# Kernel optimization log

Hardware: AMD Instinct MI355X
Metric: run time of the kernel (lower is better)

The kernel has to match this reference:

```python
import jax, jax.numpy as jnp
import numpy as np

D_MODEL = 1024
D_HEAD = 64  # d_model / num_heads
NEG_INF = -1e9  # matches torch code's -1000000000.0 additive mask


def setup_inputs() -> dict:
    key = jax.random.key(0)
    ks = jax.random.split(key, 9)
    B, S = 4, 4096
    scale = 0.02
    return {
        "q": jax.random.normal(ks[0], (B, S, D_MODEL), dtype=jnp.float32),
        "k": jax.random.normal(ks[1], (B, S, D_MODEL), dtype=jnp.float32),
        "v": jax.random.normal(ks[2], (B, S, D_MODEL), dtype=jnp.float32),
        "WQ_w": jax.random.normal(ks[3], (D_HEAD, D_MODEL), dtype=jnp.float32) * scale,
        "WQ_b": jax.random.normal(ks[4], (D_HEAD,), dtype=jnp.float32) * scale,
        "WK_w": jax.random.normal(ks[5], (D_HEAD, D_MODEL), dtype=jnp.float32) * scale,
        "WK_b": jax.random.normal(ks[6], (D_HEAD,), dtype=jnp.float32) * scale,
        "WV_w": jax.random.normal(ks[7], (D_HEAD, D_MODEL), dtype=jnp.float32) * scale,
        "WV_b": jax.random.normal(ks[8], (D_HEAD,), dtype=jnp.float32) * scale,
    }


def reference(q, k, v, WQ_w, WQ_b, WK_w, WK_b, WV_w, WV_b):
    # Linear projections (torch nn.Linear: x @ W.T + b)
    qh = jnp.einsum("bsd,hd->bsh", q, WQ_w) + WQ_b  # [B,S,64]
    kh = jnp.einsum("bsd,hd->bsh", k, WK_w) + WK_b
    vh = jnp.einsum("bsd,hd->bsh", v, WV_w) + WV_b
    # Scaled dot-product scores [B,S,S]
    scores = jnp.einsum("bqh,bkh->bqk", qh, kh) / np.sqrt(D_HEAD).astype(np.float32)
    # Causal additive mask: upper triangle (j > i) gets -1e9
    S = scores.shape[-1]
    causal = jnp.triu(jnp.ones((S, S), dtype=scores.dtype), k=1) * NEG_INF
    scores = scores + causal
    attn = jax.nn.softmax(scores, axis=-1)
    out = jnp.einsum("bqk,bkh->bqh", attn, vh)  # [B,S,64]
    # Dropout is identity in eval mode (deterministic reference)
    return out
```

## Files before the change

### kernel.cpp

```cpp
#include <hip/hip_runtime.h>

#define SEQ 4096
#define DM  1024
#define DH  64
#define NB  4
#define SLOTS_PER_B 288

typedef __attribute__((ext_vector_type(4))) float  f32x4;
typedef __attribute__((ext_vector_type(8))) __bf16 bf16x8;

__device__ __forceinline__ unsigned short f2bf(float f) {
    unsigned int u = __float_as_uint(f);
    u += 0x7FFFu + ((u >> 16) & 1u);
    return (unsigned short)(u >> 16);
}

__device__ __forceinline__ f32x4 mfma_bf16(bf16x8 a, bf16x8 b, f32x4 c) {
    return __builtin_amdgcn_mfma_f32_16x16x32_bf16(a, b, c, 0, 0, 0);
}

__global__ __launch_bounds__(256) void proj_kernel(
    const float* __restrict__ xq, const float* __restrict__ xk, const float* __restrict__ xv,
    const float* __restrict__ Wq, const float* __restrict__ bq,
    const float* __restrict__ Wk, const float* __restrict__ bk,
    const float* __restrict__ Wv, const float* __restrict__ bv,
    unsigned short* __restrict__ qh, unsigned short* __restrict__ kh,
    unsigned short* __restrict__ vhT)
{
    __shared__ unsigned short x_tile[64][72];
    __shared__ unsigned short w_tile[64][72];

    const int which = blockIdx.y;
    const float* X  = (which == 0) ? xq : (which == 1) ? xk : xv;
    const float* W  = (which == 0) ? Wq : (which == 1) ? Wk : Wv;
    const float* Bb = (which == 0) ? bq : (which == 1) ? bk : bv;

    const int m0   = blockIdx.x * 64;
    const int t    = threadIdx.x;
    const int wv   = t >> 6;
    const int lane = t & 63;
    const int quad = lane >> 4;
    const int l16  = lane & 15;
    const int sr   = t >> 2;
    const int sc   = (t & 3) << 4;

    f32x4 acc[4];
#pragma unroll
    for (int i = 0; i < 4; ++i) acc[i] = f32x4{0.f, 0.f, 0.f, 0.f};

    const float* xg = X + (size_t)(m0 + sr) * DM + sc;
    const float* wg = W + (size_t)sr * DM + sc;

    f32x4 xr[4], wr[4];
#pragma unroll
    for (int i = 0; i < 4; ++i) { xr[i] = *(const f32x4*)(xg + i * 4); wr[i] = *(const f32x4*)(wg + i * 4); }

    for (int kc = 0; kc < DM; kc += 64) {
        __syncthreads();
#pragma unroll
        for (int i = 0; i < 4; ++i) {
            *(ushort4*)&x_tile[sr][sc + i * 4] =
                make_ushort4(f2bf(xr[i][0]), f2bf(xr[i][1]), f2bf(xr[i][2]), f2bf(xr[i][3]));
            *(ushort4*)&w_tile[sr][sc + i * 4] =
                make_ushort4(f2bf(wr[i][0]), f2bf(wr[i][1]), f2bf(wr[i][2]), f2bf(wr[i][3]));
        }
        __syncthreads();
        if (kc + 64 < DM) {
            const float* xn = xg + kc + 64;
            const float* wn = wg + kc + 64;
#pragma unroll
            for (int i = 0; i < 4; ++i) { xr[i] = *(const f32x4*)(xn + i * 4); wr[i] = *(const f32x4*)(wn + i * 4); }
        }
#pragma unroll
        for (int ks = 0; ks < 2; ++ks) {
            bf16x8 a = *(const bf16x8*)&x_tile[wv * 16 + l16][ks * 32 + quad * 8];
#pragma unroll
            for (int nt = 0; nt < 4; ++nt) {
                bf16x8 b = *(const bf16x8*)&w_tile[nt * 16 + l16][ks * 32 + quad * 8];
                acc[nt] = mfma_bf16(a, b, acc[nt]);
            }
        }
    }

    __syncthreads();
#pragma unroll
    for (int nt = 0; nt < 4; ++nt) {
        float bias = Bb[nt * 16 + l16];
#pragma unroll
        for (int r = 0; r < 4; ++r)
            x_tile[wv * 16 + quad * 4 + r][nt * 16 + l16] = f2bf(acc[nt][r] + bias);
    }
    __syncthreads();

    if (which < 2) {
        unsigned short* out = (which == 0) ? qh : kh;
        unsigned short* og  = out + (size_t)(m0 + sr) * DH + sc;
        *(int4*)og       = *(const int4*)&x_tile[sr][sc];
        *(int4*)(og + 8) = *(const int4*)&x_tile[sr][sc + 8];
    } else {
        const int bb = m0 >> 12;
        const int s0 = m0 & 4095;
        const int h  = sr;
        const int r0 = sc;
        __align__(16) unsigned short tmp[16];
#pragma unroll
        for (int i = 0; i < 16; ++i) tmp[i] = x_tile[r0 + i][h];
        unsigned short* og = vhT + (size_t)bb * DH * SEQ + (size_t)h * SEQ + (s0 + r0);
        *(int4*)og       = *(const int4*)&tmp[0];
        *(int4*)(og + 8) = *(const int4*)&tmp[8];
    }
}

__global__ __launch_bounds__(256) void attn_split_kernel(
    const unsigned short* __restrict__ qh, const unsigned short* __restrict__ kh,
    const unsigned short* __restrict__ vhT,
    float* __restrict__ pO, float* __restrict__ pm, float* __restrict__ pl)
{
    const int chunk = blockIdx.x;
    const int qt    = blockIdx.y;
    const int b     = blockIdx.z;
    const int nc    = (qt + 8) >> 3;
    if (chunk >= nc) return;

    const int g = qt >> 3, rr = qt & 7;
    const int slot = b * SLOTS_PER_B + 4 * g * (g + 1) + rr * (g + 1) + chunk;
    const int c0 = chunk * 8;
    const int c1 = min(c0 + 8, qt + 1);

    __shared__ unsigned short k_t[64][72];
    __shared__ unsigned short v_t[64][72];
    __shared__ unsigned short qp[64][72];

    const int t    = threadIdx.x;
    const int wv   = t >> 6;
    const int lane = t & 63;
    const int quad = lane >> 4;
    const int l16  = lane & 15;
    const int sr   = t >> 2;
    const int sc   = (t & 3) << 4;

    const size_t base = (size_t)b * SEQ * DH;

    {
        const unsigned short* gq = qh + base + (size_t)(qt * 64 + sr) * DH + sc;
        *(int4*)&qp[sr][sc]     = *(const int4*)gq;
        *(int4*)&qp[sr][sc + 8] = *(const int4*)(gq + 8);
    }
    __syncthreads();
    bf16x8 qfrag[2];
    qfrag[0] = *(const bf16x8*)&qp[wv * 16 + l16][quad * 8];
    qfrag[1] = *(const bf16x8*)&qp[wv * 16 + l16][32 + quad * 8];

    f32x4 o_acc[4];
#pragma unroll
    for (int i = 0; i < 4; ++i) o_acc[i] = f32x4{0.f, 0.f, 0.f, 0.f};
    float m_i[4], l_i[4];
#pragma unroll
    for (int r = 0; r < 4; ++r) { m_i[r] = -1e30f; l_i[r] = 0.f; }

    const int rowb = wv * 16 + quad * 4;

    for (int jt = c0; jt < c1; ++jt) {
        __syncthreads();
        {
            const unsigned short* kg = kh + base + (size_t)(jt * 64 + sr) * DH + sc;
            *(int4*)&k_t[sr][sc]     = *(const int4*)kg;
            *(int4*)&k_t[sr][sc + 8] = *(const int4*)(kg + 8);
            const unsigned short* vg = vhT + (size_t)b * DH * SEQ + (size_t)sr * SEQ + (jt * 64 + sc);
            *(int4*)&v_t[sr][sc]     = *(const int4*)vg;
            *(int4*)&v_t[sr][sc + 8] = *(const int4*)(vg + 8);
        }
        __syncthreads();

        f32x4 s_acc[4];
#pragma unroll
        for (int i = 0; i < 4; ++i) s_acc[i] = f32x4{0.f, 0.f, 0.f, 0.f};
#pragma unroll
        for (int ks = 0; ks < 2; ++ks) {
#pragma unroll
            for (int nt = 0; nt < 4; ++nt) {
                bf16x8 bfr = *(const bf16x8*)&k_t[nt * 16 + l16][ks * 32 + quad * 8];
                s_acc[nt] = mfma_bf16(qfrag[ks], bfr, s_acc[nt]);
            }
        }

        const bool diag = (jt == qt);
#pragma unroll
        for (int nt = 0; nt < 4; ++nt) {
            const int col = nt * 16 + l16;
#pragma unroll
            for (int r = 0; r < 4; ++r) {
                float sv = s_acc[nt][r] * 0.125f;
                if (diag && (col > rowb + r)) sv = -1e30f;
                s_acc[nt][r] = sv;
            }
        }

        float mx[4];
#pragma unroll
        for (int r = 0; r < 4; ++r)
            mx[r] = fmaxf(fmaxf(s_acc[0][r], s_acc[1][r]), fmaxf(s_acc[2][r], s_acc[3][r]));
#pragma unroll
        for (int off = 1; off < 16; off <<= 1)
#pragma unroll
            for (int r = 0; r < 4; ++r)
                mx[r] = fmaxf(mx[r], __shfl_xor(mx[r], off, 64));

        float alpha[4];
#pragma unroll
        for (int r = 0; r < 4; ++r) {
            float mn = fmaxf(m_i[r], mx[r]);
            alpha[r] = __expf(m_i[r] - mn);
            m_i[r]   = mn;
        }

        float rs[4] = {0.f, 0.f, 0.f, 0.f};
#pragma unroll
        for (int nt = 0; nt < 4; ++nt)
#pragma unroll
            for (int r = 0; r < 4; ++r) {
                float p = __expf(s_acc[nt][r] - m_i[r]);
                s_acc[nt][r] = p;
                rs[r] += p;
            }
#pragma unroll
        for (int off = 1; off < 16; off <<= 1)
#pragma unroll
            for (int r = 0; r < 4; ++r)
                rs[r] += __shfl_xor(rs[r], off, 64);
#pragma unroll
        for (int r = 0; r < 4; ++r) l_i[r] = l_i[r] * alpha[r] + rs[r];

#pragma unroll
        for (int nt = 0; nt < 4; ++nt)
#pragma unroll
            for (int r = 0; r < 4; ++r)
                qp[rowb + r][nt * 16 + l16] = f2bf(s_acc[nt][r]);

#pragma unroll
        for (int nt = 0; nt < 4; ++nt)
#pragma unroll
            for (int r = 0; r < 4; ++r)
                o_acc[nt][r] *= alpha[r];

#pragma unroll
        for (int ks = 0; ks < 2; ++ks) {
            bf16x8 pa = *(const bf16x8*)&qp[wv * 16 + l16][ks * 32 + quad * 8];
#pragma unroll
            for (int nt = 0; nt < 4; ++nt) {
                bf16x8 vb = *(const bf16x8*)&v_t[nt * 16 + l16][ks * 32 + quad * 8];
                o_acc[nt] = mfma_bf16(pa, vb, o_acc[nt]);
            }
        }
    }

    float* po = pO + (size_t)slot * 4096;
#pragma unroll
    for (int nt = 0; nt < 4; ++nt)
#pragma unroll
        for (int r = 0; r < 4; ++r)
            po[(rowb + r) * 64 + nt * 16 + l16] = o_acc[nt][r];
    if (l16 == 0) {
#pragma unroll
        for (int r = 0; r < 4; ++r) {
            pm[slot * 64 + rowb + r] = m_i[r];
            pl[slot * 64 + rowb + r] = l_i[r];
        }
    }
}

__global__ __launch_bounds__(256) void attn_merge_kernel(
    const float* __restrict__ pO, const float* __restrict__ pm, const float* __restrict__ pl,
    float* __restrict__ out)
{
    const int qt = blockIdx.x;
    const int b  = blockIdx.y;
    const int nc = (qt + 8) >> 3;
    const int g = qt >> 3, rr = qt & 7;
    const int s0 = b * SLOTS_PER_B + 4 * g * (g + 1) + rr * (g + 1);

    const int t   = threadIdx.x;
    const int row = t >> 2;
    const int c0  = (t & 3) << 4;

    float mstar = -1e30f;
    for (int c = 0; c < nc; ++c)
        mstar = fmaxf(mstar, pm[(s0 + c) * 64 + row]);

    f32x4 acc[4];
#pragma unroll
    for (int i = 0; i < 4; ++i) acc[i] = f32x4{0.f, 0.f, 0.f, 0.f};
    float lsum = 0.f;

    for (int c = 0; c < nc; ++c) {
        const float w = __expf(pm[(s0 + c) * 64 + row] - mstar);
        lsum += w * pl[(s0 + c) * 64 + row];
        const float* p = pO + (size_t)(s0 + c) * 4096 + row * 64 + c0;
#pragma unroll
        for (int i = 0; i < 4; ++i) {
            f32x4 v = *(const f32x4*)(p + i * 4);
            acc[i] += w * v;
        }
    }

    const float inv = 1.0f / lsum;
    float* og = out + (size_t)b * SEQ * DH + (size_t)(qt * 64 + row) * DH + c0;
#pragma unroll
    for (int i = 0; i < 4; ++i)
        *(f32x4*)(og + i * 4) = acc[i] * inv;
}

extern "C" void kernel_launch(void* const* d_in, const int* in_sizes, int n_in,
                              void* d_out, int out_size, void* d_ws, size_t ws_size,
                              hipStream_t stream)
{
    (void)in_sizes; (void)n_in; (void)out_size; (void)ws_size;
    const float* q  = (const float*)d_in[0];
    const float* k  = (const float*)d_in[1];
    const float* v  = (const float*)d_in[2];
    const float* Wq = (const float*)d_in[3];
    const float* bq = (const float*)d_in[4];
    const float* Wk = (const float*)d_in[5];
    const float* bk = (const float*)d_in[6];
    const float* Wv = (const float*)d_in[7];
    const float* bv = (const float*)d_in[8];
    float* out = (float*)d_out;

    unsigned short* qh  = (unsigned short*)d_ws;
    unsigned short* kh  = qh + (size_t)NB * SEQ * DH;
    unsigned short* vhT = kh + (size_t)NB * SEQ * DH;
    float* pO = (float*)(vhT + (size_t)NB * SEQ * DH);
    float* pm = pO + (size_t)NB * SLOTS_PER_B * 4096;
    float* pl = pm + (size_t)NB * SLOTS_PER_B * 64;

    proj_kernel<<<dim3(NB * SEQ / 64, 3), 256, 0, stream>>>(
        q, k, v, Wq, bq, Wk, bk, Wv, bv, qh, kh, vhT);
    attn_split_kernel<<<dim3(8, SEQ / 64, NB), 256, 0, stream>>>(qh, kh, vhT, pO, pm, pl);
    attn_merge_kernel<<<dim3(SEQ / 64, NB), 256, 0, stream>>>(pO, pm, pl, out);
}
```

Measured before the change: 280.5 us.

## Prepack bf16 weights and double-buffer projection GEMM with async LDS loads

Adds a small pre-kernel that converts the three projection weight matrices to bf16 once, already laid out in MFMA fragment order, into scratch space that the attention partials reuse later. The projection kernel then streams these weight fragments straight into LDS with global_load_lds into double-buffered tiles, and keeps X fp32 loads several chunks ahead in registers. This removes the redundant per-block weight fp32 loads and conversions and overlaps memory with MFMA. In exchange it adds an extra kernel launch, manual waitcnt/barrier bookkeeping, and higher LDS and register use.

```diff
diff --git a/kernel.cpp b/kernel.cpp
--- a/kernel.cpp
+++ b/kernel.cpp
@@ -15,25 +15,56 @@
     return (unsigned short)(u >> 16);
 }
 
+__device__ __forceinline__ unsigned short bfc(float f) {
+    __bf16 h = (__bf16)f;
+    return __builtin_bit_cast(unsigned short, h);
+}
+
 __device__ __forceinline__ f32x4 mfma_bf16(bf16x8 a, bf16x8 b, f32x4 c) {
     return __builtin_amdgcn_mfma_f32_16x16x32_bf16(a, b, c, 0, 0, 0);
 }
 
+__device__ __forceinline__ void gload_lds16(const void* g, void* l) {
+    __builtin_amdgcn_global_load_lds(
+        (const __attribute__((address_space(1))) void*)g,
+        (__attribute__((address_space(3))) void*)l, 16, 0, 0);
+}
+
+__global__ __launch_bounds__(256) void wprep_kernel(
+    const float* __restrict__ Wq, const float* __restrict__ Wk, const float* __restrict__ Wv,
+    unsigned short* __restrict__ Wf)
+{
+    const int which = blockIdx.y;
+    const int kc    = blockIdx.x;
+    const float* W  = (which == 0) ? Wq : (which == 1) ? Wk : Wv;
+    unsigned short* out = Wf + (size_t)which * 65536 + (size_t)kc * 4096;
+    const int t = threadIdx.x;
+#pragma unroll
+    for (int s = t; s < 512; s += 256) {
+        const int ks = s >> 8, nt = (s >> 6) & 3, ln = s & 63;
+        const int qd = ln >> 4, l = ln & 15;
+        const float* src = W + (size_t)(nt * 16 + l) * DM + kc * 64 + ks * 32 + qd * 8;
+        f32x4 v0 = *(const f32x4*)src;
+        f32x4 v1 = *(const f32x4*)(src + 4);
+        *(ushort4*)(out + (size_t)s * 8)     = make_ushort4(bfc(v0[0]), bfc(v0[1]), bfc(v0[2]), bfc(v0[3]));
+        *(ushort4*)(out + (size_t)s * 8 + 4) = make_ushort4(bfc(v1[0]), bfc(v1[1]), bfc(v1[2]), bfc(v1[3]));
+    }
+}
+
 __global__ __launch_bounds__(256) void proj_kernel(
     const float* __restrict__ xq, const float* __restrict__ xk, const float* __restrict__ xv,
-    const float* __restrict__ Wq, const float* __restrict__ bq,
-    const float* __restrict__ Wk, const float* __restrict__ bk,
-    const float* __restrict__ Wv, const float* __restrict__ bv,
+    const unsigned short* __restrict__ Wf,
+    const float* __restrict__ bq, const float* __restrict__ bk, const float* __restrict__ bv,
     unsigned short* __restrict__ qh, unsigned short* __restrict__ kh,
     unsigned short* __restrict__ vhT)
 {
-    __shared__ unsigned short x_tile[64][72];
-    __shared__ unsigned short w_tile[64][72];
+    __shared__ unsigned short x_t[2][64][72];
+    __shared__ unsigned short wfb[2][4096];
 
     const int which = blockIdx.y;
     const float* X  = (which == 0) ? xq : (which == 1) ? xk : xv;
-    const float* W  = (which == 0) ? Wq : (which == 1) ? Wk : Wv;
     const float* Bb = (which == 0) ? bq : (which == 1) ? bk : bv;
+    const unsigned short* Wg = Wf + (size_t)which * 65536;
 
     const int m0   = blockIdx.x * 64;
     const int t    = threadIdx.x;
@@ -49,54 +80,82 @@
     for (int i = 0; i < 4; ++i) acc[i] = f32x4{0.f, 0.f, 0.f, 0.f};
 
     const float* xg = X + (size_t)(m0 + sr) * DM + sc;
-    const float* wg = W + (size_t)sr * DM + sc;
-
-    f32x4 xr[4], wr[4];
-#pragma unroll
-    for (int i = 0; i < 4; ++i) { xr[i] = *(const f32x4*)(xg + i * 4); wr[i] = *(const f32x4*)(wg + i * 4); }
-
-    for (int kc = 0; kc < DM; kc += 64) {
-        __syncthreads();
-#pragma unroll
-        for (int i = 0; i < 4; ++i) {
-            *(ushort4*)&x_tile[sr][sc + i * 4] =
-                make_ushort4(f2bf(xr[i][0]), f2bf(xr[i][1]), f2bf(xr[i][2]), f2bf(xr[i][3]));
-            *(ushort4*)&w_tile[sr][sc + i * 4] =
-                make_ushort4(f2bf(wr[i][0]), f2bf(wr[i][1]), f2bf(wr[i][2]), f2bf(wr[i][3]));
-        }
-        __syncthreads();
-        if (kc + 64 < DM) {
-            const float* xn = xg + kc + 64;
-            const float* wn = wg + kc + 64;
-#pragma unroll
-            for (int i = 0; i < 4; ++i) { xr[i] = *(const f32x4*)(xn + i * 4); wr[i] = *(const f32x4*)(wn + i * 4); }
-        }
-#pragma unroll
-        for (int ks = 0; ks < 2; ++ks) {
-            bf16x8 a = *(const bf16x8*)&x_tile[wv * 16 + l16][ks * 32 + quad * 8];
-#pragma unroll
-            for (int nt = 0; nt < 4; ++nt) {
-                bf16x8 b = *(const bf16x8*)&w_tile[nt * 16 + l16][ks * 32 + quad * 8];
-                acc[nt] = mfma_bf16(a, b, acc[nt]);
+
+    f32x4 xr[2][4];
+#pragma unroll
+    for (int i = 0; i < 4; ++i) xr[0][i] = *(const f32x4*)(xg + i * 4);
+#pragma unroll
+    for (int i = 0; i < 4; ++i) xr[1][i] = *(const f32x4*)(xg + 64 + i * 4);
+    {
+        const unsigned short* gs = Wg + (wv * 2) * 512 + lane * 8;
+        gload_lds16(gs,       &wfb[0][(wv * 2) * 512]);
+        gload_lds16(gs + 512, &wfb[0][(wv * 2) * 512 + 512]);
+    }
+    __builtin_amdgcn_sched_barrier(0);
+#pragma unroll
+    for (int i = 0; i < 4; ++i) {
+        f32x4 v = xr[0][i];
+        *(ushort4*)&x_t[0][sr][sc + i * 4] =
+            make_ushort4(bfc(v[0]), bfc(v[1]), bfc(v[2]), bfc(v[3]));
+    }
+#pragma unroll
+    for (int i = 0; i < 4; ++i) xr[0][i] = *(const f32x4*)(xg + 128 + i * 4);
+    asm volatile("s_waitcnt vmcnt(4)" ::: "memory");
+    asm volatile("s_waitcnt lgkmcnt(0)" ::: "memory");
+    __builtin_amdgcn_s_barrier();
+
+#pragma unroll
+    for (int j = 0; j < 16; ++j) {
+        const int cur = j & 1, nxt = cur ^ 1;
+        if (j + 1 < 16) {
+#pragma unroll
+            for (int i = 0; i < 4; ++i) {
+                f32x4 v = xr[nxt][i];
+                *(ushort4*)&x_t[nxt][sr][sc + i * 4] =
+                    make_ushort4(bfc(v[0]), bfc(v[1]), bfc(v[2]), bfc(v[3]));
             }
-        }
-    }
-
-    __syncthreads();
+            const unsigned short* gs = Wg + (size_t)(j + 1) * 4096 + (wv * 2) * 512 + lane * 8;
+            gload_lds16(gs,       &wfb[nxt][(wv * 2) * 512]);
+            gload_lds16(gs + 512, &wfb[nxt][(wv * 2) * 512 + 512]);
+        }
+        __builtin_amdgcn_sched_barrier(0);
+        if (j + 3 < 16) {
+            const float* xn = xg + (j + 3) * 64;
+#pragma unroll
+            for (int i = 0; i < 4; ++i) xr[nxt][i] = *(const f32x4*)(xn + i * 4);
+        }
+        bf16x8 a0 = *(const bf16x8*)&x_t[cur][wv * 16 + l16][quad * 8];
+        bf16x8 a1 = *(const bf16x8*)&x_t[cur][wv * 16 + l16][32 + quad * 8];
+#pragma unroll
+        for (int nt = 0; nt < 4; ++nt) {
+            bf16x8 b0 = *(const bf16x8*)&wfb[cur][(nt * 64 + lane) * 8];
+            acc[nt] = mfma_bf16(a0, b0, acc[nt]);
+        }
+#pragma unroll
+        for (int nt = 0; nt < 4; ++nt) {
+            bf16x8 b1 = *(const bf16x8*)&wfb[cur][((4 + nt) * 64 + lane) * 8];
+            acc[nt] = mfma_bf16(a1, b1, acc[nt]);
+        }
+        if (j < 13) asm volatile("s_waitcnt vmcnt(4)" ::: "memory");
+        else        asm volatile("s_waitcnt vmcnt(0)" ::: "memory");
+        asm volatile("s_waitcnt lgkmcnt(0)" ::: "memory");
+        __builtin_amdgcn_s_barrier();
+    }
+
 #pragma unroll
     for (int nt = 0; nt < 4; ++nt) {
         float bias = Bb[nt * 16 + l16];
 #pragma unroll
         for (int r = 0; r < 4; ++r)
-            x_tile[wv * 16 + quad * 4 + r][nt * 16 + l16] = f2bf(acc[nt][r] + bias);
+            x_t[0][wv * 16 + quad * 4 + r][nt * 16 + l16] = f2bf(acc[nt][r] + bias);
     }
     __syncthreads();
 
     if (which < 2) {
         unsigned short* out = (which == 0) ? qh : kh;
         unsigned short* og  = out + (size_t)(m0 + sr) * DH + sc;
-        *(int4*)og       = *(const int4*)&x_tile[sr][sc];
-        *(int4*)(og + 8) = *(const int4*)&x_tile[sr][sc + 8];
+        *(int4*)og       = *(const int4*)&x_t[0][sr][sc];
+        *(int4*)(og + 8) = *(const int4*)&x_t[0][sr][sc + 8];
     } else {
         const int bb = m0 >> 12;
         const int s0 = m0 & 4095;
@@ -104,7 +163,7 @@
         const int r0 = sc;
         __align__(16) unsigned short tmp[16];
 #pragma unroll
-        for (int i = 0; i < 16; ++i) tmp[i] = x_tile[r0 + i][h];
+        for (int i = 0; i < 16; ++i) tmp[i] = x_t[0][r0 + i][h];
         unsigned short* og = vhT + (size_t)bb * DH * SEQ + (size_t)h * SEQ + (s0 + r0);
         *(int4*)og       = *(const int4*)&tmp[0];
         *(int4*)(og + 8) = *(const int4*)&tmp[8];
@@ -332,9 +391,11 @@
     float* pO = (float*)(vhT + (size_t)NB * SEQ * DH);
     float* pm = pO + (size_t)NB * SLOTS_PER_B * 4096;
     float* pl = pm + (size_t)NB * SLOTS_PER_B * 64;
-
+    unsigned short* Wfb = (unsigned short*)pO;
+
+    wprep_kernel<<<dim3(16, 3), 256, 0, stream>>>(Wq, Wk, Wv, Wfb);
     proj_kernel<<<dim3(NB * SEQ / 64, 3), 256, 0, stream>>>(
-        q, k, v, Wq, bq, Wk, bk, Wv, bv, qh, kh, vhT);
+        q, k, v, Wfb, bq, bk, bv, qh, kh, vhT);
     attn_split_kernel<<<dim3(8, SEQ / 64, NB), 256, 0, stream>>>(qh, kh, vhT, pO, pm, pl);
     attn_merge_kernel<<<dim3(SEQ / 64, NB), 256, 0, stream>>>(pO, pm, pl, out);
 }
```

Result: no change. 283.3 us (+1.0%).

## Pre-swizzle bf16 weights and stream X directly into MFMA fragments in projection

Applied to the files above, without the earlier changes.

Adds a small kernel that converts the three projection weight matrices to bf16 once per call, laid out in MFMA fragment order, reusing the pO workspace before the split kernel overwrites it. The projection kernel then drops its shared-memory staging and barriers: each wave loads its X rows straight from global memory, converts them in registers, and reads the pre-swizzled weights directly. The merge kernel is split across four times more blocks, each thread handling one f32x4, to raise parallelism. In exchange, weight fragments are re-read from global or cache by every block, and it adds one more launch.

```diff
diff --git a/kernel.cpp b/kernel.cpp
--- a/kernel.cpp
+++ b/kernel.cpp
@@ -15,25 +15,56 @@
     return (unsigned short)(u >> 16);
 }
 
+__device__ __forceinline__ unsigned short bfc(float f) {
+    __bf16 h = (__bf16)f;
+    return __builtin_bit_cast(unsigned short, h);
+}
+
+__device__ __forceinline__ bf16x8 cvt8(f32x4 lo, f32x4 hi) {
+    bf16x8 r;
+    r[0] = (__bf16)lo[0]; r[1] = (__bf16)lo[1]; r[2] = (__bf16)lo[2]; r[3] = (__bf16)lo[3];
+    r[4] = (__bf16)hi[0]; r[5] = (__bf16)hi[1]; r[6] = (__bf16)hi[2]; r[7] = (__bf16)hi[3];
+    return r;
+}
+
 __device__ __forceinline__ f32x4 mfma_bf16(bf16x8 a, bf16x8 b, f32x4 c) {
     return __builtin_amdgcn_mfma_f32_16x16x32_bf16(a, b, c, 0, 0, 0);
 }
 
+__global__ __launch_bounds__(256) void wprep_kernel(
+    const float* __restrict__ Wq, const float* __restrict__ Wk, const float* __restrict__ Wv,
+    unsigned short* __restrict__ Wf)
+{
+    const int which = blockIdx.y;
+    const int kc    = blockIdx.x;
+    const float* W  = (which == 0) ? Wq : (which == 1) ? Wk : Wv;
+    unsigned short* out = Wf + (size_t)which * 65536 + (size_t)kc * 4096;
+    const int t = threadIdx.x;
+#pragma unroll
+    for (int s = t; s < 512; s += 256) {
+        const int ks = s >> 8, nt = (s >> 6) & 3, ln = s & 63;
+        const int qd = ln >> 4, l = ln & 15;
+        const float* src = W + (size_t)(nt * 16 + l) * DM + kc * 64 + ks * 32 + qd * 8;
+        f32x4 v0 = *(const f32x4*)src;
+        f32x4 v1 = *(const f32x4*)(src + 4);
+        *(ushort4*)(out + (size_t)s * 8)     = make_ushort4(bfc(v0[0]), bfc(v0[1]), bfc(v0[2]), bfc(v0[3]));
+        *(ushort4*)(out + (size_t)s * 8 + 4) = make_ushort4(bfc(v1[0]), bfc(v1[1]), bfc(v1[2]), bfc(v1[3]));
+    }
+}
+
 __global__ __launch_bounds__(256) void proj_kernel(
     const float* __restrict__ xq, const float* __restrict__ xk, const float* __restrict__ xv,
-    const float* __restrict__ Wq, const float* __restrict__ bq,
-    const float* __restrict__ Wk, const float* __restrict__ bk,
-    const float* __restrict__ Wv, const float* __restrict__ bv,
+    const unsigned short* __restrict__ Wf,
+    const float* __restrict__ bq, const float* __restrict__ bk, const float* __restrict__ bv,
     unsigned short* __restrict__ qh, unsigned short* __restrict__ kh,
     unsigned short* __restrict__ vhT)
 {
-    __shared__ unsigned short x_tile[64][72];
-    __shared__ unsigned short w_tile[64][72];
+    __shared__ unsigned short ot[4][16][72];
 
     const int which = blockIdx.y;
     const float* X  = (which == 0) ? xq : (which == 1) ? xk : xv;
-    const float* W  = (which == 0) ? Wq : (which == 1) ? Wk : Wv;
     const float* Bb = (which == 0) ? bq : (which == 1) ? bk : bv;
+    const unsigned short* Wg = Wf + (size_t)which * 65536;
 
     const int m0   = blockIdx.x * 64;
     const int t    = threadIdx.x;
@@ -41,71 +72,78 @@
     const int lane = t & 63;
     const int quad = lane >> 4;
     const int l16  = lane & 15;
-    const int sr   = t >> 2;
-    const int sc   = (t & 3) << 4;
+
+    const int row = m0 + wv * 16 + l16;
+    const float* xrow = X + (size_t)row * DM + quad * 8;
+    const unsigned short* wb = Wg + lane * 8;
 
     f32x4 acc[4];
 #pragma unroll
     for (int i = 0; i < 4; ++i) acc[i] = f32x4{0.f, 0.f, 0.f, 0.f};
 
-    const float* xg = X + (size_t)(m0 + sr) * DM + sc;
-    const float* wg = W + (size_t)sr * DM + sc;
-
-    f32x4 xr[4], wr[4];
-#pragma unroll
-    for (int i = 0; i < 4; ++i) { xr[i] = *(const f32x4*)(xg + i * 4); wr[i] = *(const f32x4*)(wg + i * 4); }
-
-    for (int kc = 0; kc < DM; kc += 64) {
-        __syncthreads();
-#pragma unroll
-        for (int i = 0; i < 4; ++i) {
-            *(ushort4*)&x_tile[sr][sc + i * 4] =
-                make_ushort4(f2bf(xr[i][0]), f2bf(xr[i][1]), f2bf(xr[i][2]), f2bf(xr[i][3]));
-            *(ushort4*)&w_tile[sr][sc + i * 4] =
-                make_ushort4(f2bf(wr[i][0]), f2bf(wr[i][1]), f2bf(wr[i][2]), f2bf(wr[i][3]));
-        }
-        __syncthreads();
-        if (kc + 64 < DM) {
-            const float* xn = xg + kc + 64;
-            const float* wn = wg + kc + 64;
-#pragma unroll
-            for (int i = 0; i < 4; ++i) { xr[i] = *(const f32x4*)(xn + i * 4); wr[i] = *(const f32x4*)(wn + i * 4); }
-        }
-#pragma unroll
-        for (int ks = 0; ks < 2; ++ks) {
-            bf16x8 a = *(const bf16x8*)&x_tile[wv * 16 + l16][ks * 32 + quad * 8];
-#pragma unroll
-            for (int nt = 0; nt < 4; ++nt) {
-                bf16x8 b = *(const bf16x8*)&w_tile[nt * 16 + l16][ks * 32 + quad * 8];
-                acc[nt] = mfma_bf16(a, b, acc[nt]);
-            }
-        }
-    }
-
-    __syncthreads();
+    f32x4 xa0 = *(const f32x4*)(xrow);
+    f32x4 xa1 = *(const f32x4*)(xrow + 4);
+    f32x4 xa2 = *(const f32x4*)(xrow + 32);
+    f32x4 xa3 = *(const f32x4*)(xrow + 36);
+
+#pragma unroll
+    for (int kc = 0; kc < 16; ++kc) {
+        bf16x8 b0 = *(const bf16x8*)(wb + (size_t)kc * 4096);
+        bf16x8 b1 = *(const bf16x8*)(wb + (size_t)kc * 4096 + 512);
+        bf16x8 b2 = *(const bf16x8*)(wb + (size_t)kc * 4096 + 1024);
+        bf16x8 b3 = *(const bf16x8*)(wb + (size_t)kc * 4096 + 1536);
+        bf16x8 b4 = *(const bf16x8*)(wb + (size_t)kc * 4096 + 2048);
+        bf16x8 b5 = *(const bf16x8*)(wb + (size_t)kc * 4096 + 2560);
+        bf16x8 b6 = *(const bf16x8*)(wb + (size_t)kc * 4096 + 3072);
+        bf16x8 b7 = *(const bf16x8*)(wb + (size_t)kc * 4096 + 3584);
+
+        f32x4 xn0, xn1, xn2, xn3;
+        if (kc < 15) {
+            const float* xp = xrow + (kc + 1) * 64;
+            xn0 = *(const f32x4*)(xp);
+            xn1 = *(const f32x4*)(xp + 4);
+            xn2 = *(const f32x4*)(xp + 32);
+            xn3 = *(const f32x4*)(xp + 36);
+        }
+
+        bf16x8 a0 = cvt8(xa0, xa1);
+        bf16x8 a1 = cvt8(xa2, xa3);
+
+        acc[0] = mfma_bf16(a0, b0, acc[0]);
+        acc[1] = mfma_bf16(a0, b1, acc[1]);
+        acc[2] = mfma_bf16(a0, b2, acc[2]);
+        acc[3] = mfma_bf16(a0, b3, acc[3]);
+        acc[0] = mfma_bf16(a1, b4, acc[0]);
+        acc[1] = mfma_bf16(a1, b5, acc[1]);
+        acc[2] = mfma_bf16(a1, b6, acc[2]);
+        acc[3] = mfma_bf16(a1, b7, acc[3]);
+
+        if (kc < 15) { xa0 = xn0; xa1 = xn1; xa2 = xn2; xa3 = xn3; }
+    }
+
 #pragma unroll
     for (int nt = 0; nt < 4; ++nt) {
         float bias = Bb[nt * 16 + l16];
 #pragma unroll
         for (int r = 0; r < 4; ++r)
-            x_tile[wv * 16 + quad * 4 + r][nt * 16 + l16] = f2bf(acc[nt][r] + bias);
-    }
-    __syncthreads();
+            ot[wv][quad * 4 + r][nt * 16 + l16] = f2bf(acc[nt][r] + bias);
+    }
+    asm volatile("s_waitcnt lgkmcnt(0)" ::: "memory");
 
     if (which < 2) {
-        unsigned short* out = (which == 0) ? qh : kh;
-        unsigned short* og  = out + (size_t)(m0 + sr) * DH + sc;
-        *(int4*)og       = *(const int4*)&x_tile[sr][sc];
-        *(int4*)(og + 8) = *(const int4*)&x_tile[sr][sc + 8];
+        unsigned short* outp = (which == 0) ? qh : kh;
+        const int r2 = lane >> 2;
+        const int c2 = (lane & 3) << 4;
+        unsigned short* og = outp + (size_t)(m0 + wv * 16 + r2) * DH + c2;
+        *(int4*)og       = *(const int4*)&ot[wv][r2][c2];
+        *(int4*)(og + 8) = *(const int4*)&ot[wv][r2][c2 + 8];
     } else {
         const int bb = m0 >> 12;
-        const int s0 = m0 & 4095;
-        const int h  = sr;
-        const int r0 = sc;
+        const int s0 = (m0 & 4095) + wv * 16;
         __align__(16) unsigned short tmp[16];
 #pragma unroll
-        for (int i = 0; i < 16; ++i) tmp[i] = x_tile[r0 + i][h];
-        unsigned short* og = vhT + (size_t)bb * DH * SEQ + (size_t)h * SEQ + (s0 + r0);
+        for (int i = 0; i < 16; ++i) tmp[i] = ot[wv][i][lane];
+        unsigned short* og = vhT + (size_t)bb * DH * SEQ + (size_t)lane * SEQ + s0;
         *(int4*)og       = *(const int4*)&tmp[0];
         *(int4*)(og + 8) = *(const int4*)&tmp[8];
     }
@@ -275,39 +313,32 @@
 {
     const int qt = blockIdx.x;
     const int b  = blockIdx.y;
+    const int rq = blockIdx.z;
     const int nc = (qt + 8) >> 3;
     const int g = qt >> 3, rr = qt & 7;
     const int s0 = b * SLOTS_PER_B + 4 * g * (g + 1) + rr * (g + 1);
 
     const int t   = threadIdx.x;
-    const int row = t >> 2;
-    const int c0  = (t & 3) << 4;
+    const int row = rq * 16 + (t >> 4);
+    const int c0  = (t & 15) << 2;
 
     float mstar = -1e30f;
     for (int c = 0; c < nc; ++c)
         mstar = fmaxf(mstar, pm[(s0 + c) * 64 + row]);
 
-    f32x4 acc[4];
-#pragma unroll
-    for (int i = 0; i < 4; ++i) acc[i] = f32x4{0.f, 0.f, 0.f, 0.f};
+    f32x4 acc = f32x4{0.f, 0.f, 0.f, 0.f};
     float lsum = 0.f;
 
     for (int c = 0; c < nc; ++c) {
         const float w = __expf(pm[(s0 + c) * 64 + row] - mstar);
         lsum += w * pl[(s0 + c) * 64 + row];
-        const float* p = pO + (size_t)(s0 + c) * 4096 + row * 64 + c0;
-#pragma unroll
-        for (int i = 0; i < 4; ++i) {
-            f32x4 v = *(const f32x4*)(p + i * 4);
-            acc[i] += w * v;
-        }
+        f32x4 v = *(const f32x4*)(pO + (size_t)(s0 + c) * 4096 + row * 64 + c0);
+        acc += w * v;
     }
 
     const float inv = 1.0f / lsum;
     float* og = out + (size_t)b * SEQ * DH + (size_t)(qt * 64 + row) * DH + c0;
-#pragma unroll
-    for (int i = 0; i < 4; ++i)
-        *(f32x4*)(og + i * 4) = acc[i] * inv;
+    *(f32x4*)og = acc * inv;
 }
 
 extern "C" void kernel_launch(void* const* d_in, const int* in_sizes, int n_in,
@@ -332,9 +363,11 @@
     float* pO = (float*)(vhT + (size_t)NB * SEQ * DH);
     float* pm = pO + (size_t)NB * SLOTS_PER_B * 4096;
     float* pl = pm + (size_t)NB * SLOTS_PER_B * 64;
-
+    unsigned short* Wfb = (unsigned short*)pO;
+
+    wprep_kernel<<<dim3(16, 3), 256, 0, stream>>>(Wq, Wk, Wv, Wfb);
     proj_kernel<<<dim3(NB * SEQ / 64, 3), 256, 0, stream>>>(
-        q, k, v, Wq, bq, Wk, bk, Wv, bv, qh, kh, vhT);
+        q, k, v, Wfb, bq, bk, bv, qh, kh, vhT);
     attn_split_kernel<<<dim3(8, SEQ / 64, NB), 256, 0, stream>>>(qh, kh, vhT, pO, pm, pl);
-    attn_merge_kernel<<<dim3(SEQ / 64, NB), 256, 0, stream>>>(pO, pm, pl, out);
-}
+    attn_merge_kernel<<<dim3(SEQ / 64, NB, 4), 256, 0, stream>>>(pO, pm, pl, out);
+}
```

Measured after the change: 288.2 us. 1.03x slower.
